# Kernel tuning notes

Hardware: AMD Instinct MI355X
Metric: run time of the kernel (lower is better)

## Reference

```python
import jax, jax.numpy as jnp
import numpy as np

D = 1024
R = 64
B = 8
S = 4096


def setup_inputs() -> dict:
    key = jax.random.key(0)
    kx, kq = jax.random.split(key)
    x = jax.random.normal(kx, (B, S, D), dtype=jnp.float32)
    # matches torch init: 0.1 * randn(d, r)
    Q = 0.1 * jax.random.normal(kq, (D, R), dtype=jnp.float32)
    return {"x": x, "Q": Q}


def reference(x, Q):
    d = x.shape[-1]
    scale = jnp.float32(1.0 / np.sqrt(d))
    # shared low-rank projection: Q == K
    xQ = jnp.einsum('imk,kl->iml', x, Q * scale)          # [B, S, R]
    scores = jax.nn.softmax(jnp.einsum('iml,inl->imn', xQ, xQ), axis=-1)  # [B, S, S]
    yhat = jnp.einsum('imn,inj->imj', scores, x)          # [B, S, D], V = x
    return yhat
```

## Files before the change

kernel.cpp:

```cpp
#include <hip/hip_runtime.h>

#define DD 1024
#define RR 64
#define BB 8
#define SS 4096
#define KB 64

typedef __attribute__((ext_vector_type(8))) short short8;
typedef __attribute__((ext_vector_type(4))) float f32x4;

__device__ inline unsigned short f2bf(float f){
  unsigned int u = __float_as_uint(f);
  unsigned int r = (u + 0x7fffu + ((u >> 16) & 1u)) >> 16;
  return (unsigned short)r;
}

__global__ __launch_bounds__(256) void k0_qt(const float* __restrict__ Q,
                                             unsigned short* __restrict__ Qt){
  __shared__ float lds[64 * 65];
  int d0 = blockIdx.x * 64;
  int tid = threadIdx.x;
  const float scale = 0.03125f;
#pragma unroll
  for (int k = 0; k < 16; k++){
    int idx = tid + 256 * k; int r = idx >> 6, c = idx & 63;
    lds[r * 65 + c] = Q[(d0 + r) * 64 + c] * scale;
  }
  __syncthreads();
#pragma unroll
  for (int k = 0; k < 16; k++){
    int idx = tid + 256 * k; int c = idx >> 6, r = idx & 63;
    Qt[c * 1024 + d0 + r] = f2bf(lds[r * 65 + c]);
  }
}

__global__ __launch_bounds__(256) void k1_xq(const float* __restrict__ x,
                                             const unsigned short* __restrict__ Qt,
                                             unsigned short* __restrict__ xq){
  int tid = threadIdx.x;
  int w = tid >> 6, l = tid & 63;
  int l15 = l & 15, lh = l >> 4;
  int r0 = blockIdx.x * 128 + w * 32;
  f32x4 acc[2][4];
#pragma unroll
  for (int i = 0; i < 2; i++)
#pragma unroll
    for (int j = 0; j < 4; j++) acc[i][j] = (f32x4)0.0f;

  for (int step = 0; step < 32; step++){
    int dbase = step * 32 + lh * 8;
    short8 a[2];
#pragma unroll
    for (int mt = 0; mt < 2; mt++){
      const float* px = x + (long)(r0 + 16 * mt + l15) * DD + dbase;
      float4 f0 = *reinterpret_cast<const float4*>(px);
      float4 f1 = *reinterpret_cast<const float4*>(px + 4);
      short8 t;
      t[0] = (short)f2bf(f0.x); t[1] = (short)f2bf(f0.y);
      t[2] = (short)f2bf(f0.z); t[3] = (short)f2bf(f0.w);
      t[4] = (short)f2bf(f1.x); t[5] = (short)f2bf(f1.y);
      t[6] = (short)f2bf(f1.z); t[7] = (short)f2bf(f1.w);
      a[mt] = t;
    }
#pragma unroll
    for (int nt = 0; nt < 4; nt++){
      short8 bfr = *reinterpret_cast<const short8*>(Qt + (16 * nt + l15) * 1024 + dbase);
      acc[0][nt] = __builtin_amdgcn_mfma_f32_16x16x32_bf16(a[0], bfr, acc[0][nt], 0, 0, 0);
      acc[1][nt] = __builtin_amdgcn_mfma_f32_16x16x32_bf16(a[1], bfr, acc[1][nt], 0, 0, 0);
    }
  }
#pragma unroll
  for (int mt = 0; mt < 2; mt++)
#pragma unroll
    for (int nt = 0; nt < 4; nt++)
#pragma unroll
      for (int reg = 0; reg < 4; reg++){
        long row = r0 + 16 * mt + 4 * lh + reg;
        int col = 16 * nt + l15;
        xq[row * RR + col] = f2bf(acc[mt][nt][reg]);
      }
}

__global__ __launch_bounds__(256) void k1_xt(const float* __restrict__ x,
                                             unsigned short* __restrict__ xt){
  __shared__ float lds[64 * 65];
  int bid = blockIdx.x;
  int st = bid & 63, dt = (bid >> 6) & 15, b = bid >> 10;
  int s0 = st * 64, d0 = dt * 64;
  int tid = threadIdx.x;
  const float* xb = x + (long)b * SS * DD;
#pragma unroll
  for (int k = 0; k < 16; k++){
    int idx = tid + 256 * k; int r = idx >> 6, c = idx & 63;
    lds[r * 65 + c] = xb[(long)(s0 + r) * DD + d0 + c];
  }
  __syncthreads();
  unsigned short* xtb = xt + (long)b * DD * SS;
#pragma unroll
  for (int k = 0; k < 16; k++){
    int idx = tid + 256 * k; int dd = idx >> 6, rr = idx & 63;
    xtb[(long)(d0 + dd) * SS + s0 + rr] = f2bf(lds[rr * 65 + dd]);
  }
}

__global__ __launch_bounds__(512) void k2_stats(const unsigned short* __restrict__ xq,
                                                float* __restrict__ invl){
  int tid = threadIdx.x; int w = tid >> 6, l = tid & 63;
  int l15 = l & 15, lh = l >> 4;
  int bid = blockIdx.x; int b = bid >> 5; int q0 = (bid & 31) * 128 + w * 16;
  long qrow = (long)b * SS + q0;
  short8 a[2];
#pragma unroll
  for (int ks = 0; ks < 2; ks++)
    a[ks] = *reinterpret_cast<const short8*>(xq + (qrow + l15) * RR + 32 * ks + 8 * lh);
  float lsum[4] = {0.f, 0.f, 0.f, 0.f};
  const unsigned short* xk = xq + (long)b * SS * RR;
  for (int kt = 0; kt < SS / 16; kt++){
    f32x4 c = (f32x4)0.0f;
#pragma unroll
    for (int ks = 0; ks < 2; ks++){
      short8 bfr = *reinterpret_cast<const short8*>(xk + (long)(kt * 16 + l15) * RR + 32 * ks + 8 * lh);
      c = __builtin_amdgcn_mfma_f32_16x16x32_bf16(a[ks], bfr, c, 0, 0, 0);
    }
#pragma unroll
    for (int reg = 0; reg < 4; reg++) lsum[reg] += __expf(c[reg]);
  }
#pragma unroll
  for (int m = 1; m < 16; m <<= 1)
#pragma unroll
    for (int reg = 0; reg < 4; reg++) lsum[reg] += __shfl_xor(lsum[reg], m, 64);
  if (l15 == 0){
#pragma unroll
    for (int reg = 0; reg < 4; reg++)
      invl[qrow + 4 * lh + reg] = 1.0f / lsum[reg];
  }
}

__global__ __launch_bounds__(512, 2) void k3_pv(const unsigned short* __restrict__ xq,
                                                const unsigned short* __restrict__ xt,
                                                const float* __restrict__ invl,
                                                float* __restrict__ out){
  __shared__ unsigned short Vt[256 * 72];
  __shared__ unsigned short Pl[2][64 * 72];
  int tid = threadIdx.x; int w = tid >> 6, l = tid & 63;
  int l15 = l & 15, lh = l >> 4;
  int wr = w >> 2, wc = w & 3;
  int bid = blockIdx.x;
  int qt = bid & 31, dc = (bid >> 5) & 3, b = bid >> 7;
  int q0 = qt * 128, d0 = dc * 256;
  long qrow = (long)b * SS + q0 + 64 * wr;
  const unsigned short* xqb = xq + (long)b * SS * RR;
  const unsigned short* xtb = xt + ((long)b * DD + d0) * SS;

  short8 qa[4][2];
#pragma unroll
  for (int mt = 0; mt < 4; mt++)
#pragma unroll
    for (int ks = 0; ks < 2; ks++)
      qa[mt][ks] = *reinterpret_cast<const short8*>(xq + (qrow + 16 * mt + l15) * RR + 32 * ks + 8 * lh);

  float il[4][4];
#pragma unroll
  for (int mt = 0; mt < 4; mt++)
#pragma unroll
    for (int reg = 0; reg < 4; reg++)
      il[mt][reg] = invl[qrow + 16 * mt + 4 * lh + reg];

  f32x4 acc[4][4];
#pragma unroll
  for (int i = 0; i < 4; i++)
#pragma unroll
    for (int j = 0; j < 4; j++) acc[i][j] = (f32x4)0.0f;

  for (int kt = 0; kt < SS / KB; kt++){
    __syncthreads();
#pragma unroll
    for (int it = 0; it < 4; it++){
      int i = tid + 512 * it;
      int dl = i >> 3, k8 = i & 7;
      short8 v = *reinterpret_cast<const short8*>(xtb + (long)dl * SS + kt * KB + k8 * 8);
      *reinterpret_cast<short8*>(&Vt[dl * 72 + k8 * 8]) = v;
    }
    f32x4 c[4];
#pragma unroll
    for (int mt = 0; mt < 4; mt++) c[mt] = (f32x4)0.0f;
#pragma unroll
    for (int ks = 0; ks < 2; ks++){
      short8 kb = *reinterpret_cast<const short8*>(xqb + (long)(kt * KB + 16 * wc + l15) * RR + 32 * ks + 8 * lh);
#pragma unroll
      for (int mt = 0; mt < 4; mt++)
        c[mt] = __builtin_amdgcn_mfma_f32_16x16x32_bf16(qa[mt][ks], kb, c[mt], 0, 0, 0);
    }
#pragma unroll
    for (int mt = 0; mt < 4; mt++)
#pragma unroll
      for (int reg = 0; reg < 4; reg++){
        int row = 16 * mt + 4 * lh + reg;
        int key = 16 * wc + l15;
        Pl[wr][row * 72 + key] = f2bf(__expf(c[mt][reg]));
      }
    __syncthreads();
#pragma unroll
    for (int ks = 0; ks < 2; ks++){
      short8 pa[4], vb[4];
#pragma unroll
      for (int mt = 0; mt < 4; mt++)
        pa[mt] = *reinterpret_cast<const short8*>(&Pl[wr][(16 * mt + l15) * 72 + 32 * ks + 8 * lh]);
#pragma unroll
      for (int nt = 0; nt < 4; nt++)
        vb[nt] = *reinterpret_cast<const short8*>(&Vt[(64 * wc + 16 * nt + l15) * 72 + 32 * ks + 8 * lh]);
#pragma unroll
      for (int mt = 0; mt < 4; mt++)
#pragma unroll
        for (int nt = 0; nt < 4; nt++)
          acc[mt][nt] = __builtin_amdgcn_mfma_f32_16x16x32_bf16(pa[mt], vb[nt], acc[mt][nt], 0, 0, 0);
    }
  }
#pragma unroll
  for (int mt = 0; mt < 4; mt++)
#pragma unroll
    for (int nt = 0; nt < 4; nt++)
#pragma unroll
      for (int reg = 0; reg < 4; reg++){
        long row = qrow + 16 * mt + 4 * lh + reg;
        int col = d0 + 64 * wc + 16 * nt + l15;
        out[row * DD + col] = acc[mt][nt][reg] * il[mt][reg];
      }
}

extern "C" void kernel_launch(void* const* d_in, const int* in_sizes, int n_in,
                              void* d_out, int out_size, void* d_ws, size_t ws_size,
                              hipStream_t stream){
  const float* x = (const float*)d_in[0];
  const float* Q = (const float*)d_in[1];
  float* out = (float*)d_out;
  char* ws = (char*)d_ws;
  unsigned short* Qt   = (unsigned short*)(ws);
  unsigned short* xqp  = (unsigned short*)(ws + 131072);
  float*          invl = (float*)(ws + 131072 + 4194304);
  unsigned short* xt   = (unsigned short*)(ws + 131072 + 4194304 + 131072);

  hipLaunchKernelGGL(k0_qt,    dim3(16),   dim3(256), 0, stream, Q, Qt);
  hipLaunchKernelGGL(k1_xq,    dim3(256),  dim3(256), 0, stream, x, Qt, xqp);
  hipLaunchKernelGGL(k1_xt,    dim3(8192), dim3(256), 0, stream, x, xt);
  hipLaunchKernelGGL(k2_stats, dim3(256),  dim3(512), 0, stream, xqp, invl);
  hipLaunchKernelGGL(k3_pv,    dim3(1024), dim3(512), 0, stream, xqp, xt, invl, out);
}
```

Baseline: 930.7 us.

## Fuse softmax row-sum into PV kernel with register-resident P and double-buffered V

Drops the separate stats kernel and accumulates the softmax denominators inside the PV kernel, normalizing at the end. The score MFMA is transposed so exp'd P stays in registers as the B operand, which removes the P round-trip through LDS and one barrier per tile. V tiles are double-buffered in XOR-swizzled LDS with a register prefetch of the next tile, and outputs are written as vector stores. No max subtraction is added, the same as before. The trade-off is higher register pressure from the wider 2x8 accumulator tile and the prefetch registers.

```diff
diff --git a/kernel.cpp b/kernel.cpp
--- a/kernel.cpp
+++ b/kernel.cpp
@@ -4,7 +4,6 @@
 #define RR 64
 #define BB 8
 #define SS 4096
-#define KB 64
 
 typedef __attribute__((ext_vector_type(8))) short short8;
 typedef __attribute__((ext_vector_type(4))) float f32x4;
@@ -103,129 +102,131 @@
   }
 }
 
-__global__ __launch_bounds__(512) void k2_stats(const unsigned short* __restrict__ xq,
-                                                float* __restrict__ invl){
-  int tid = threadIdx.x; int w = tid >> 6, l = tid & 63;
-  int l15 = l & 15, lh = l >> 4;
-  int bid = blockIdx.x; int b = bid >> 5; int q0 = (bid & 31) * 128 + w * 16;
-  long qrow = (long)b * SS + q0;
-  short8 a[2];
-#pragma unroll
-  for (int ks = 0; ks < 2; ks++)
-    a[ks] = *reinterpret_cast<const short8*>(xq + (qrow + l15) * RR + 32 * ks + 8 * lh);
-  float lsum[4] = {0.f, 0.f, 0.f, 0.f};
-  const unsigned short* xk = xq + (long)b * SS * RR;
-  for (int kt = 0; kt < SS / 16; kt++){
-    f32x4 c = (f32x4)0.0f;
-#pragma unroll
-    for (int ks = 0; ks < 2; ks++){
-      short8 bfr = *reinterpret_cast<const short8*>(xk + (long)(kt * 16 + l15) * RR + 32 * ks + 8 * lh);
-      c = __builtin_amdgcn_mfma_f32_16x16x32_bf16(a[ks], bfr, c, 0, 0, 0);
-    }
-#pragma unroll
-    for (int reg = 0; reg < 4; reg++) lsum[reg] += __expf(c[reg]);
-  }
-#pragma unroll
-  for (int m = 1; m < 16; m <<= 1)
-#pragma unroll
-    for (int reg = 0; reg < 4; reg++) lsum[reg] += __shfl_xor(lsum[reg], m, 64);
-  if (l15 == 0){
-#pragma unroll
-    for (int reg = 0; reg < 4; reg++)
-      invl[qrow + 4 * lh + reg] = 1.0f / lsum[reg];
-  }
-}
-
 __global__ __launch_bounds__(512, 2) void k3_pv(const unsigned short* __restrict__ xq,
                                                 const unsigned short* __restrict__ xt,
-                                                const float* __restrict__ invl,
                                                 float* __restrict__ out){
-  __shared__ unsigned short Vt[256 * 72];
-  __shared__ unsigned short Pl[2][64 * 72];
-  int tid = threadIdx.x; int w = tid >> 6, l = tid & 63;
+  __shared__ __align__(16) unsigned short Vt[2][256 * 64];
+  int tid = threadIdx.x, w = tid >> 6, l = tid & 63;
   int l15 = l & 15, lh = l >> 4;
-  int wr = w >> 2, wc = w & 3;
+  int qg = w & 3, dg = w >> 2;
   int bid = blockIdx.x;
   int qt = bid & 31, dc = (bid >> 5) & 3, b = bid >> 7;
   int q0 = qt * 128, d0 = dc * 256;
-  long qrow = (long)b * SS + q0 + 64 * wr;
   const unsigned short* xqb = xq + (long)b * SS * RR;
   const unsigned short* xtb = xt + ((long)b * DD + d0) * SS;
-
-  short8 qa[4][2];
-#pragma unroll
-  for (int mt = 0; mt < 4; mt++)
+  long qrow = (long)b * SS + q0 + 32 * qg;
+
+  short8 qb[2][2];
+#pragma unroll
+  for (int qf = 0; qf < 2; qf++)
 #pragma unroll
     for (int ks = 0; ks < 2; ks++)
-      qa[mt][ks] = *reinterpret_cast<const short8*>(xq + (qrow + 16 * mt + l15) * RR + 32 * ks + 8 * lh);
-
-  float il[4][4];
-#pragma unroll
-  for (int mt = 0; mt < 4; mt++)
-#pragma unroll
-    for (int reg = 0; reg < 4; reg++)
-      il[mt][reg] = invl[qrow + 16 * mt + 4 * lh + reg];
-
-  f32x4 acc[4][4];
-#pragma unroll
-  for (int i = 0; i < 4; i++)
-#pragma unroll
-    for (int j = 0; j < 4; j++) acc[i][j] = (f32x4)0.0f;
-
-  for (int kt = 0; kt < SS / KB; kt++){
+      qb[qf][ks] = *reinterpret_cast<const short8*>(xq + (qrow + 16 * qf + l15) * RR + 32 * ks + 8 * lh);
+
+  int koff[4];
+#pragma unroll
+  for (int kf = 0; kf < 4; kf++)
+    koff[kf] = 32 * (kf >> 1) + 4 * (kf & 1) + 8 * (l15 >> 2) + (l15 & 3);
+
+  f32x4 acc[2][8];
+#pragma unroll
+  for (int qf = 0; qf < 2; qf++)
+#pragma unroll
+    for (int nt = 0; nt < 8; nt++) acc[qf][nt] = (f32x4)0.0f;
+  float lsum[2] = {0.f, 0.f};
+
+  long ssrc[4]; int sdst[4];
+#pragma unroll
+  for (int it = 0; it < 4; it++){
+    int i = tid + 512 * it; int r = i >> 3, c = i & 7;
+    ssrc[it] = (long)r * SS + c * 8;
+    sdst[it] = r * 64 + ((c * 8) ^ ((r & 7) << 3));
+  }
+
+  short8 vreg[4];
+#pragma unroll
+  for (int it = 0; it < 4; it++) vreg[it] = *reinterpret_cast<const short8*>(xtb + ssrc[it]);
+#pragma unroll
+  for (int it = 0; it < 4; it++) *reinterpret_cast<short8*>(&Vt[0][sdst[it]]) = vreg[it];
+
+  for (int kt = 0; kt < 64; ++kt){
+    int cur = kt & 1;
+    short8 ka[4][2];
+#pragma unroll
+    for (int kf = 0; kf < 4; kf++)
+#pragma unroll
+      for (int ks = 0; ks < 2; ks++)
+        ka[kf][ks] = *reinterpret_cast<const short8*>(xqb + (long)(kt * 64 + koff[kf]) * RR + 32 * ks + 8 * lh);
     __syncthreads();
-#pragma unroll
-    for (int it = 0; it < 4; it++){
-      int i = tid + 512 * it;
-      int dl = i >> 3, k8 = i & 7;
-      short8 v = *reinterpret_cast<const short8*>(xtb + (long)dl * SS + kt * KB + k8 * 8);
-      *reinterpret_cast<short8*>(&Vt[dl * 72 + k8 * 8]) = v;
-    }
-    f32x4 c[4];
-#pragma unroll
-    for (int mt = 0; mt < 4; mt++) c[mt] = (f32x4)0.0f;
-#pragma unroll
-    for (int ks = 0; ks < 2; ks++){
-      short8 kb = *reinterpret_cast<const short8*>(xqb + (long)(kt * KB + 16 * wc + l15) * RR + 32 * ks + 8 * lh);
-#pragma unroll
-      for (int mt = 0; mt < 4; mt++)
-        c[mt] = __builtin_amdgcn_mfma_f32_16x16x32_bf16(qa[mt][ks], kb, c[mt], 0, 0, 0);
-    }
-#pragma unroll
-    for (int mt = 0; mt < 4; mt++)
-#pragma unroll
-      for (int reg = 0; reg < 4; reg++){
-        int row = 16 * mt + 4 * lh + reg;
-        int key = 16 * wc + l15;
-        Pl[wr][row * 72 + key] = f2bf(__expf(c[mt][reg]));
-      }
-    __syncthreads();
-#pragma unroll
-    for (int ks = 0; ks < 2; ks++){
-      short8 pa[4], vb[4];
-#pragma unroll
-      for (int mt = 0; mt < 4; mt++)
-        pa[mt] = *reinterpret_cast<const short8*>(&Pl[wr][(16 * mt + l15) * 72 + 32 * ks + 8 * lh]);
-#pragma unroll
-      for (int nt = 0; nt < 4; nt++)
-        vb[nt] = *reinterpret_cast<const short8*>(&Vt[(64 * wc + 16 * nt + l15) * 72 + 32 * ks + 8 * lh]);
-#pragma unroll
-      for (int mt = 0; mt < 4; mt++)
-#pragma unroll
-        for (int nt = 0; nt < 4; nt++)
-          acc[mt][nt] = __builtin_amdgcn_mfma_f32_16x16x32_bf16(pa[mt], vb[nt], acc[mt][nt], 0, 0, 0);
-    }
-  }
-#pragma unroll
-  for (int mt = 0; mt < 4; mt++)
-#pragma unroll
-    for (int nt = 0; nt < 4; nt++)
-#pragma unroll
-      for (int reg = 0; reg < 4; reg++){
-        long row = qrow + 16 * mt + 4 * lh + reg;
-        int col = d0 + 64 * wc + 16 * nt + l15;
-        out[row * DD + col] = acc[mt][nt][reg] * il[mt][reg];
-      }
+    if (kt < 63){
+#pragma unroll
+      for (int it = 0; it < 4; it++)
+        vreg[it] = *reinterpret_cast<const short8*>(xtb + ssrc[it] + (long)(kt + 1) * 64);
+    }
+    f32x4 cacc[2][4];
+#pragma unroll
+    for (int qf = 0; qf < 2; qf++)
+#pragma unroll
+      for (int kf = 0; kf < 4; kf++){
+        f32x4 c = (f32x4)0.0f;
+        c = __builtin_amdgcn_mfma_f32_16x16x32_bf16(ka[kf][0], qb[qf][0], c, 0, 0, 0);
+        c = __builtin_amdgcn_mfma_f32_16x16x32_bf16(ka[kf][1], qb[qf][1], c, 0, 0, 0);
+        cacc[qf][kf] = c;
+      }
+    short8 pb[2][2];
+#pragma unroll
+    for (int qf = 0; qf < 2; qf++){
+#pragma unroll
+      for (int ks = 0; ks < 2; ks++){
+        short8 t;
+#pragma unroll
+        for (int r = 0; r < 4; r++){
+          float p = __expf(cacc[qf][2 * ks][r]);
+          lsum[qf] += p; t[r] = (short)f2bf(p);
+        }
+#pragma unroll
+        for (int r = 0; r < 4; r++){
+          float p = __expf(cacc[qf][2 * ks + 1][r]);
+          lsum[qf] += p; t[4 + r] = (short)f2bf(p);
+        }
+        pb[qf][ks] = t;
+      }
+    }
+#pragma unroll
+    for (int nt = 0; nt < 8; nt++){
+      int row = 128 * dg + 16 * nt + l15;
+#pragma unroll
+      for (int ks = 0; ks < 2; ks++){
+        short8 va = *reinterpret_cast<const short8*>(
+            &Vt[cur][row * 64 + ((32 * ks + 8 * lh) ^ ((l15 & 7) << 3))]);
+        acc[0][nt] = __builtin_amdgcn_mfma_f32_16x16x32_bf16(va, pb[0][ks], acc[0][nt], 0, 0, 0);
+        acc[1][nt] = __builtin_amdgcn_mfma_f32_16x16x32_bf16(va, pb[1][ks], acc[1][nt], 0, 0, 0);
+      }
+    }
+    if (kt < 63){
+#pragma unroll
+      for (int it = 0; it < 4; it++) *reinterpret_cast<short8*>(&Vt[cur ^ 1][sdst[it]]) = vreg[it];
+    }
+  }
+
+  float il[2];
+#pragma unroll
+  for (int qf = 0; qf < 2; qf++){
+    float s = lsum[qf];
+    s += __shfl_xor(s, 16, 64);
+    s += __shfl_xor(s, 32, 64);
+    il[qf] = 1.0f / s;
+  }
+#pragma unroll
+  for (int qf = 0; qf < 2; qf++){
+    long row = qrow + 16 * qf + l15;
+#pragma unroll
+    for (int nt = 0; nt < 8; nt++){
+      f32x4 o = acc[qf][nt] * il[qf];
+      int col = d0 + 128 * dg + 16 * nt + 4 * lh;
+      *reinterpret_cast<f32x4*>(out + row * DD + col) = o;
+    }
+  }
 }
 
 extern "C" void kernel_launch(void* const* d_in, const int* in_sizes, int n_in,
@@ -235,14 +236,12 @@
   const float* Q = (const float*)d_in[1];
   float* out = (float*)d_out;
   char* ws = (char*)d_ws;
-  unsigned short* Qt   = (unsigned short*)(ws);
-  unsigned short* xqp  = (unsigned short*)(ws + 131072);
-  float*          invl = (float*)(ws + 131072 + 4194304);
-  unsigned short* xt   = (unsigned short*)(ws + 131072 + 4194304 + 131072);
-
-  hipLaunchKernelGGL(k0_qt,    dim3(16),   dim3(256), 0, stream, Q, Qt);
-  hipLaunchKernelGGL(k1_xq,    dim3(256),  dim3(256), 0, stream, x, Qt, xqp);
-  hipLaunchKernelGGL(k1_xt,    dim3(8192), dim3(256), 0, stream, x, xt);
-  hipLaunchKernelGGL(k2_stats, dim3(256),  dim3(512), 0, stream, xqp, invl);
-  hipLaunchKernelGGL(k3_pv,    dim3(1024), dim3(512), 0, stream, xqp, xt, invl, out);
-}
+  unsigned short* Qt  = (unsigned short*)(ws);
+  unsigned short* xqp = (unsigned short*)(ws + 131072);
+  unsigned short* xt  = (unsigned short*)(ws + 131072 + 4194304);
+
+  hipLaunchKernelGGL(k0_qt,  dim3(16),   dim3(256), 0, stream, Q, Qt);
+  hipLaunchKernelGGL(k1_xq,  dim3(256),  dim3(256), 0, stream, x, Qt, xqp);
+  hipLaunchKernelGGL(k1_xt,  dim3(8192), dim3(256), 0, stream, x, xt);
+  hipLaunchKernelGGL(k3_pv,  dim3(1024), dim3(512), 0, stream, xqp, xt, out);
+}
```

New measurement: 875.7 us. 1.06x faster.
